# Performance work log

Hardware: AMD Instinct MI355X
Metric: run time of the kernel (lower is better)

The kernel has to match this reference:

```python
import jax, jax.numpy as jnp
import numpy as np

B, S, D, H = 4, 2048, 1024, 16
HD = D // H  # 64


def setup_inputs() -> dict:
    key = jax.random.key(0)
    ks = jax.random.split(key, 5)
    s = 1.0 / np.sqrt(D)
    return {
        "x": jax.random.normal(ks[0], (B, S, D), dtype=jnp.float32),
        "W_attn": jax.random.normal(ks[1], (D, 3 * D), dtype=jnp.float32) * s,
        "b_attn": jnp.zeros((3 * D,), dtype=jnp.float32),
        "W_proj": jax.random.normal(ks[2], (D, D), dtype=jnp.float32) * s,
        "b_proj": jnp.zeros((D,), dtype=jnp.float32),
    }


def reference(x, W_attn, b_attn, W_proj, b_proj):
    Bx, Sx, Dx = x.shape
    qkv = x @ W_attn + b_attn                      # [B,S,3D]
    q, k, v = jnp.split(qkv, 3, axis=-1)
    q = q.reshape(Bx, Sx, H, HD).transpose(0, 2, 1, 3)  # [B,H,S,hd]
    k = k.reshape(Bx, Sx, H, HD).transpose(0, 2, 1, 3)
    v = v.reshape(Bx, Sx, H, HD).transpose(0, 2, 1, 3)
    att = jnp.einsum('bhqd,bhkd->bhqk', q, k) * (HD ** -0.5)
    causal = jnp.tril(jnp.ones((Sx, Sx), dtype=bool))
    att = jnp.where(causal[None, None], att, -jnp.inf)
    att = jax.nn.softmax(att, axis=-1)
    y = jnp.einsum('bhqk,bhkd->bhqd', att, v)      # [B,H,S,hd]
    y = y.transpose(0, 2, 1, 3).reshape(Bx, Sx, Dx)
    return y @ W_proj + b_proj
```

## Files before the change

### kernel.cpp

```cpp
#include <hip/hip_runtime.h>
#include <hip/hip_bf16.h>
#include <math.h>


typedef __bf16 bf16;
typedef __bf16 bf16x8 __attribute__((ext_vector_type(8)));
typedef __bf16 bf16x4 __attribute__((ext_vector_type(4)));
typedef float f32x4 __attribute__((ext_vector_type(4)));

#define B_ 4
#define S_ 2048
#define D_ 1024
#define H_ 16
#define HD_ 64
#define QSCALE 0.1803368801f

#if __has_builtin(__builtin_amdgcn_exp2f)
#define EXP2F(x) __builtin_amdgcn_exp2f(x)
#else
#define EXP2F(x) exp2f(x)
#endif
#if __has_builtin(__builtin_amdgcn_rcpf)
#define RCPF(x) __builtin_amdgcn_rcpf(x)
#else
#define RCPF(x) (1.0f / (x))
#endif

#define GLOAD_LDS16(gptr, lptr)                                              \
    __builtin_amdgcn_global_load_lds(                                        \
        (const __attribute__((address_space(1))) void*)(uintptr_t)(gptr),    \
        (__attribute__((address_space(3))) void*)(uintptr_t)(lptr), 16, 0, 0)

__global__ void k_cvt(const float* __restrict__ in, bf16* __restrict__ out, int n) {
    int i = (blockIdx.x * 256 + threadIdx.x) * 4;
    if (i >= n) return;
    float4 v = *reinterpret_cast<const float4*>(in + i);
    bf16x4 o;
    o.x = (bf16)v.x; o.y = (bf16)v.y; o.z = (bf16)v.z; o.w = (bf16)v.w;
    *reinterpret_cast<bf16x4*>(out + i) = o;
}

__global__ void k_transpose_cvt(const float* __restrict__ W, bf16* __restrict__ WT,
                                int K, int N) {
    __shared__ float t[32][33];
    int n0 = blockIdx.x * 32, k0 = blockIdx.y * 32;
    int tx = threadIdx.x & 31, ty = threadIdx.x >> 5;
#pragma unroll
    for (int j = 0; j < 32; j += 8)
        t[ty + j][tx] = W[(size_t)(k0 + ty + j) * N + n0 + tx];
    __syncthreads();
#pragma unroll
    for (int j = 0; j < 32; j += 8)
        WT[(size_t)(n0 + ty + j) * K + k0 + tx] = (bf16)t[tx][ty + j];
}

template <int MODE>
__global__ __launch_bounds__(256) void k_gemm(
    const bf16* __restrict__ A, const bf16* __restrict__ BT,
    const float* __restrict__ bias,
    void* out0, void* out1, void* out2, int M, int N, int K) {
    __shared__ __align__(16) bf16 Asm[128 * 32];
    __shared__ __align__(16) bf16 Bsm[128 * 32];
    int mb = blockIdx.y * 128, nb = blockIdx.x * 128;
    int tid = threadIdx.x;
    int w = tid >> 6, lane = tid & 63, lo = lane & 15, qu = lane >> 4;
    int wm = (w >> 1) * 64, wn = (w & 1) * 64;
    int srow_in_wave = lane >> 2;
    int schunk = lane & 3;
    f32x4 zero = {0.f, 0.f, 0.f, 0.f};
    f32x4 acc[4][4];
#pragma unroll
    for (int i = 0; i < 4; i++)
#pragma unroll
        for (int j = 0; j < 4; j++) acc[i][j] = zero;

    int fswz = (lo >> 1) & 3;

    for (int kb = 0; kb < K; kb += 32) {
        __syncthreads();
#pragma unroll
        for (int u = 0; u < 2; u++) {
            int row0 = w * 32 + u * 16;
            int row = row0 + srow_in_wave;
            int cg = schunk ^ ((row >> 1) & 3);
            GLOAD_LDS16(A + (size_t)(mb + row) * K + kb + cg * 8, &Asm[row0 * 32]);
            GLOAD_LDS16(BT + (size_t)(nb + row) * K + kb + cg * 8, &Bsm[row0 * 32]);
        }
        __syncthreads();
        bf16x8 af[4], bfr[4];
#pragma unroll
        for (int t = 0; t < 4; t++) {
            af[t]  = *reinterpret_cast<const bf16x8*>(
                &Asm[(wm + t * 16 + lo) * 32 + (qu ^ fswz) * 8]);
            bfr[t] = *reinterpret_cast<const bf16x8*>(
                &Bsm[(wn + t * 16 + lo) * 32 + (qu ^ fswz) * 8]);
        }
#pragma unroll
        for (int i = 0; i < 4; i++)
#pragma unroll
            for (int j = 0; j < 4; j++)
                acc[i][j] = __builtin_amdgcn_mfma_f32_16x16x32_bf16(af[i], bfr[j],
                                                                    acc[i][j], 0, 0, 0);
    }
#pragma unroll
    for (int i = 0; i < 4; i++) {
#pragma unroll
        for (int j = 0; j < 4; j++) {
            int col = nb + wn + j * 16 + lo;
            float bv = bias[col];
            float v4v[4];
#pragma unroll
            for (int r = 0; r < 4; r++) v4v[r] = acc[i][j][r] + bv;
            int row0 = mb + wm + i * 16 + qu * 4;
            if (MODE == 0) {
                int b = row0 >> 11, s0 = row0 & 2047;
                int which = col >> 10, rem = col & 1023;
                int h = rem >> 6, d = rem & 63;
                int bh = b * H_ + h;
                if (which == 2) {
                    bf16x4 pk;
#pragma unroll
                    for (int r = 0; r < 4; r++) pk[r] = (bf16)v4v[r];
                    *reinterpret_cast<bf16x4*>(
                        (bf16*)out2 + ((size_t)bh * HD_ + d) * S_ + s0) = pk;
                } else {
                    bf16* dst = which == 0 ? (bf16*)out0 : (bf16*)out1;
                    float sc = which == 0 ? QSCALE : 1.0f;
#pragma unroll
                    for (int r = 0; r < 4; r++)
                        dst[((size_t)bh * S_ + s0 + r) * HD_ + d] = (bf16)(v4v[r] * sc);
                }
            } else {
#pragma unroll
                for (int r = 0; r < 4; r++)
                    ((float*)out0)[(size_t)(row0 + r) * N + col] = v4v[r];
            }
        }
    }
}

__global__ __launch_bounds__(256) void k_attn(
    const bf16* __restrict__ Q, const bf16* __restrict__ K,
    const bf16* __restrict__ Vt, bf16* __restrict__ Y) {
    __shared__ __align__(16) bf16 Ks[2][64][64];
    __shared__ __align__(16) bf16 Vs[2][64][64];
    __shared__ __align__(16) bf16 Psm[4][32][68];
    int blk = blockIdx.x;
    int bh = blk & 63;
    int p = blk >> 6;
    int tid = threadIdx.x, w = tid >> 6, lane = tid & 63;
    int lo = lane & 15, qu = lane >> 4;
    int b = bh >> 4, h = bh & 15;
    const bf16* Qb = Q + (size_t)bh * S_ * HD_;
    const bf16* Kb = K + (size_t)bh * S_ * HD_;
    const bf16* Vb = Vt + (size_t)bh * HD_ * S_;

    bf16x8 onesf;
#pragma unroll
    for (int j = 0; j < 8; j++) onesf[j] = (bf16)1.0f;

    f32x4 zero = {0.f, 0.f, 0.f, 0.f};

    int r0 = w * 16;
    int lrow = lane >> 3, lch = lane & 7;
    int gch = (lch ^ lrow) * 8;

    auto stageKV = [&](int t, int buf) {
        int kb = t * 64;
#pragma unroll
        for (int s = 0; s < 2; s++) {
            int row = r0 + s * 8;
            GLOAD_LDS16(Kb + (size_t)(kb + row + lrow) * HD_ + gch,
                        &Ks[buf][row][0]);
            GLOAD_LDS16(Vb + (size_t)(row + lrow) * S_ + kb + gch,
                        &Vs[buf][row][0]);
        }
    };

    for (int half = 0; half < 2; half++) {
        int jb = half == 0 ? 15 - p : p;
        int qbase = jb * 128 + w * 32;
        int nt = 2 * jb + 2;

        bf16x8 qf[2][2];
#pragma unroll
        for (int i = 0; i < 2; i++)
#pragma unroll
            for (int ks = 0; ks < 2; ks++)
                qf[i][ks] = *reinterpret_cast<const bf16x8*>(
                    Qb + (size_t)(qbase + i * 16 + lo) * HD_ + ks * 32 + qu * 8);

        f32x4 o[2][4];
        f32x4 lacc[2];
#pragma unroll
        for (int i = 0; i < 2; i++) {
            lacc[i] = zero;
#pragma unroll
            for (int r = 0; r < 4; r++) o[i][r] = zero;
        }

        stageKV(0, 0);

        for (int t = 0; t < nt; t++) {
            int cur = t & 1;
            if (t + 1 < nt) {
                stageKV(t + 1, cur ^ 1);
                asm volatile("s_waitcnt vmcnt(8)" ::: "memory");
            } else {
                asm volatile("s_waitcnt vmcnt(0)" ::: "memory");
            }
            __builtin_amdgcn_s_barrier();
            asm volatile("" ::: "memory");
            int kb = t * 64;
            if (kb <= qbase + 31) {
                bf16x8 kf[4][2];
#pragma unroll
                for (int kc = 0; kc < 4; kc++)
#pragma unroll
                    for (int ks = 0; ks < 2; ks++)
                        kf[kc][ks] = *reinterpret_cast<const bf16x8*>(
                            &Ks[cur][kc * 16 + lo][((ks * 4 + qu) ^ (lo & 7)) * 8]);
                f32x4 sc[2][4];
                __builtin_amdgcn_s_setprio(1);
#pragma unroll
                for (int kc = 0; kc < 4; kc++)
#pragma unroll
                    for (int i = 0; i < 2; i++) {
                        f32x4 a = __builtin_amdgcn_mfma_f32_16x16x32_bf16(
                            qf[i][0], kf[kc][0], zero, 0, 0, 0);
                        sc[i][kc] = __builtin_amdgcn_mfma_f32_16x16x32_bf16(
                            qf[i][1], kf[kc][1], a, 0, 0, 0);
                    }
                __builtin_amdgcn_s_setprio(0);
                bf16x8 vfr[4][2];
#pragma unroll
                for (int nc = 0; nc < 4; nc++)
#pragma unroll
                    for (int ks = 0; ks < 2; ks++)
                        vfr[nc][ks] = *reinterpret_cast<const bf16x8*>(
                            &Vs[cur][nc * 16 + lo][((ks * 4 + qu) ^ (lo & 7)) * 8]);
                if (kb + 63 > qbase) {
#pragma unroll
                    for (int kc = 0; kc < 4; kc++) {
                        int kj = kb + kc * 16 + lo;
#pragma unroll
                        for (int i = 0; i < 2; i++) {
                            int qi = qbase + i * 16 + qu * 4;
#pragma unroll
                            for (int r = 0; r < 4; r++)
                                sc[i][kc][r] = (kj > qi + r) ? -1e30f : sc[i][kc][r];
                        }
                    }
                }
#pragma unroll
                for (int i = 0; i < 2; i++)
#pragma unroll
                    for (int kc = 0; kc < 4; kc++)
#pragma unroll
                        for (int r = 0; r < 4; r++)
                            sc[i][kc][r] = EXP2F(sc[i][kc][r]);
#pragma unroll
                for (int i = 0; i < 2; i++)
#pragma unroll
                    for (int kc = 0; kc < 4; kc++)
#pragma unroll
                        for (int r = 0; r < 4; r++)
                            Psm[w][i * 16 + qu * 4 + r][kc * 16 + lo] =
                                (bf16)sc[i][kc][r];
                asm volatile("s_waitcnt lgkmcnt(0)" ::: "memory");
                bf16x8 pa[2][2];
#pragma unroll
                for (int i = 0; i < 2; i++)
#pragma unroll
                    for (int ks = 0; ks < 2; ks++)
                        pa[i][ks] = *reinterpret_cast<const bf16x8*>(
                            &Psm[w][i * 16 + lo][ks * 32 + qu * 8]);
                __builtin_amdgcn_s_setprio(1);
#pragma unroll
                for (int i = 0; i < 2; i++) {
                    lacc[i] = __builtin_amdgcn_mfma_f32_16x16x32_bf16(
                        pa[i][0], onesf, lacc[i], 0, 0, 0);
                    lacc[i] = __builtin_amdgcn_mfma_f32_16x16x32_bf16(
                        pa[i][1], onesf, lacc[i], 0, 0, 0);
                }
#pragma unroll
                for (int nc = 0; nc < 4; nc++)
#pragma unroll
                    for (int i = 0; i < 2; i++) {
                        o[i][nc] = __builtin_amdgcn_mfma_f32_16x16x32_bf16(
                            pa[i][0], vfr[nc][0], o[i][nc], 0, 0, 0);
                        o[i][nc] = __builtin_amdgcn_mfma_f32_16x16x32_bf16(
                            pa[i][1], vfr[nc][1], o[i][nc], 0, 0, 0);
                    }
                __builtin_amdgcn_s_setprio(0);
            }
            asm volatile("" ::: "memory");
            __builtin_amdgcn_s_barrier();
            asm volatile("" ::: "memory");
        }

#pragma unroll
        for (int i = 0; i < 2; i++) {
#pragma unroll
            for (int r = 0; r < 4; r++) {
                float inv = RCPF(lacc[i][r]);
                int s = qbase + i * 16 + qu * 4 + r;
#pragma unroll
                for (int nc = 0; nc < 4; nc++) {
                    float v = o[i][nc][r] * inv;
                    Y[((size_t)(b * S_ + s) * H_ + h) * HD_ + nc * 16 + lo] = (bf16)v;
                }
            }
        }
    }
}

extern "C" void kernel_launch(void* const* d_in, const int* in_sizes, int n_in,
                              void* d_out, int out_size, void* d_ws, size_t ws_size,
                              hipStream_t stream) {
    const float* x      = (const float*)d_in[0];
    const float* W_attn = (const float*)d_in[1];
    const float* b_attn = (const float*)d_in[2];
    const float* W_proj = (const float*)d_in[3];
    const float* b_proj = (const float*)d_in[4];
    float* out = (float*)d_out;

    char* ws = (char*)d_ws;
    size_t off = 0;
    auto alloc = [&](size_t bytes) -> void* {
        void* p = ws + off;
        off += (bytes + 255) & ~(size_t)255;
        return p;
    };
    const size_t MD = (size_t)B_ * S_ * D_;
    bf16* xb  = (bf16*)alloc(MD * 2);
    bf16* wta = (bf16*)alloc((size_t)3 * D_ * D_ * 2);
    bf16* wtp = (bf16*)alloc((size_t)D_ * D_ * 2);
    bf16* Qb  = (bf16*)alloc(MD * 2);
    bf16* Kb  = (bf16*)alloc(MD * 2);
    bf16* Vtb = (bf16*)alloc(MD * 2);
    bf16* Ya  = (bf16*)alloc(MD * 2);

    k_cvt<<<8192, 256, 0, stream>>>(x, xb, (int)MD);
    k_transpose_cvt<<<dim3(96, 32), 256, 0, stream>>>(W_attn, wta, D_, 3 * D_);
    k_transpose_cvt<<<dim3(32, 32), 256, 0, stream>>>(W_proj, wtp, D_, D_);
    k_gemm<0><<<dim3(24, 64), 256, 0, stream>>>(xb, wta, b_attn, Qb, Kb, Vtb,
                                                B_ * S_, 3 * D_, D_);
    k_attn<<<dim3(512), 256, 0, stream>>>(Qb, Kb, Vtb, Ya);
    k_gemm<1><<<dim3(8, 64), 256, 0, stream>>>(Ya, wtp, b_proj, out, nullptr, nullptr,
                                               B_ * S_, D_, D_);
}
```

Before: 267.2 us.

## Double-buffer GEMM LDS tiles with async prefetch and widen K-step to 64

The GEMM main loop now uses two LDS buffers, each widened to a 64-deep K slice. The next tile is issued via global-to-LDS loads before the current one is consumed, and the loop waits with partial vmcnt counts so memory traffic overlaps MFMA work. The XOR swizzle is reworked for the 64-wide rows, and s_setprio is raised around the MFMA block. This doubles LDS use per block, which may reduce occupancy, and relies on hand-placed waitcnt and barriers being correct.

After: 248.6 us. 7.0% less time.

```diff
diff --git a/kernel.cpp b/kernel.cpp
--- a/kernel.cpp
+++ b/kernel.cpp
@@ -59,14 +59,16 @@
     const bf16* __restrict__ A, const bf16* __restrict__ BT,
     const float* __restrict__ bias,
     void* out0, void* out1, void* out2, int M, int N, int K) {
-    __shared__ __align__(16) bf16 Asm[128 * 32];
-    __shared__ __align__(16) bf16 Bsm[128 * 32];
+    __shared__ __align__(16) bf16 Asm[2][128][64];
+    __shared__ __align__(16) bf16 Bsm[2][128][64];
     int mb = blockIdx.y * 128, nb = blockIdx.x * 128;
     int tid = threadIdx.x;
     int w = tid >> 6, lane = tid & 63, lo = lane & 15, qu = lane >> 4;
     int wm = (w >> 1) * 64, wn = (w & 1) * 64;
-    int srow_in_wave = lane >> 2;
-    int schunk = lane & 3;
+    int srow = lane >> 3, sch = lane & 7;
+    int gch = (sch ^ srow) * 8;
+    int r0 = w * 32;
+
     f32x4 zero = {0.f, 0.f, 0.f, 0.f};
     f32x4 acc[4][4];
 #pragma unroll
@@ -74,34 +76,58 @@
 #pragma unroll
         for (int j = 0; j < 4; j++) acc[i][j] = zero;
 
-    int fswz = (lo >> 1) & 3;
-
-    for (int kb = 0; kb < K; kb += 32) {
-        __syncthreads();
-#pragma unroll
-        for (int u = 0; u < 2; u++) {
-            int row0 = w * 32 + u * 16;
-            int row = row0 + srow_in_wave;
-            int cg = schunk ^ ((row >> 1) & 3);
-            GLOAD_LDS16(A + (size_t)(mb + row) * K + kb + cg * 8, &Asm[row0 * 32]);
-            GLOAD_LDS16(BT + (size_t)(nb + row) * K + kb + cg * 8, &Bsm[row0 * 32]);
-        }
-        __syncthreads();
-        bf16x8 af[4], bfr[4];
-#pragma unroll
-        for (int t = 0; t < 4; t++) {
-            af[t]  = *reinterpret_cast<const bf16x8*>(
-                &Asm[(wm + t * 16 + lo) * 32 + (qu ^ fswz) * 8]);
-            bfr[t] = *reinterpret_cast<const bf16x8*>(
-                &Bsm[(wn + t * 16 + lo) * 32 + (qu ^ fswz) * 8]);
-        }
+    const int nt = K >> 6;
+
+    auto stage = [&](int t, int buf) {
+        int kb = t * 64;
+#pragma unroll
+        for (int g = 0; g < 4; g++) {
+            int row = r0 + g * 8;
+            GLOAD_LDS16(A + (size_t)(mb + row + srow) * K + kb + gch,
+                        &Asm[buf][row][0]);
+            GLOAD_LDS16(BT + (size_t)(nb + row + srow) * K + kb + gch,
+                        &Bsm[buf][row][0]);
+        }
+    };
+
+    stage(0, 0);
+
+    for (int t = 0; t < nt; t++) {
+        int cur = t & 1;
+        if (t + 1 < nt) {
+            stage(t + 1, cur ^ 1);
+            asm volatile("s_waitcnt vmcnt(8)" ::: "memory");
+        } else {
+            asm volatile("s_waitcnt vmcnt(0)" ::: "memory");
+        }
+        __builtin_amdgcn_s_barrier();
+        asm volatile("" ::: "memory");
+        bf16x8 af[4][2], bfr[4][2];
+#pragma unroll
+        for (int tt = 0; tt < 4; tt++)
+#pragma unroll
+            for (int ks = 0; ks < 2; ks++) {
+                af[tt][ks] = *reinterpret_cast<const bf16x8*>(
+                    &Asm[cur][wm + tt * 16 + lo][((ks * 4 + qu) ^ (lo & 7)) * 8]);
+                bfr[tt][ks] = *reinterpret_cast<const bf16x8*>(
+                    &Bsm[cur][wn + tt * 16 + lo][((ks * 4 + qu) ^ (lo & 7)) * 8]);
+            }
+        __builtin_amdgcn_s_setprio(1);
 #pragma unroll
         for (int i = 0; i < 4; i++)
 #pragma unroll
-            for (int j = 0; j < 4; j++)
-                acc[i][j] = __builtin_amdgcn_mfma_f32_16x16x32_bf16(af[i], bfr[j],
-                                                                    acc[i][j], 0, 0, 0);
+            for (int j = 0; j < 4; j++) {
+                acc[i][j] = __builtin_amdgcn_mfma_f32_16x16x32_bf16(
+                    af[i][0], bfr[j][0], acc[i][j], 0, 0, 0);
+                acc[i][j] = __builtin_amdgcn_mfma_f32_16x16x32_bf16(
+                    af[i][1], bfr[j][1], acc[i][j], 0, 0, 0);
+            }
+        __builtin_amdgcn_s_setprio(0);
+        asm volatile("" ::: "memory");
+        __builtin_amdgcn_s_barrier();
+        asm volatile("" ::: "memory");
     }
+
 #pragma unroll
     for (int i = 0; i < 4; i++) {
 #pragma unroll
```
